# Performance work log

Measured on AMD Instinct MI355X. Metric: run time of the kernel, lower is better.

The kernel has to match this reference:

```python
import jax, jax.numpy as jnp
import numpy as np

N = 100000      # nodes
E = 1600000     # edges (avg degree 16)
IN_DIM = 128
OUT_DIM = 64


def setup_inputs() -> dict:
    key = jax.random.key(0)
    k0, k1, k2, k3, k4 = jax.random.split(key, 5)
    h = jax.random.normal(k0, (N, IN_DIM), dtype=jnp.float32)
    src = jax.random.randint(k1, (E,), 0, N)
    dst = jax.random.randint(k2, (E,), 0, N)
    W = jax.random.normal(k3, (OUT_DIM, IN_DIM), dtype=jnp.float32) * 0.05  # fc.weight
    a = jax.random.normal(k4, (2 * OUT_DIM,), dtype=jnp.float32) * 0.05     # attn_fc.weight (flattened)
    return {"h": h, "src": src, "dst": dst, "W": W, "a": a}


def reference(h, src, dst, W, a):
    # z = fc(h)
    z = h @ W.T                                   # [N, OUT_DIM]
    # attn_fc([z_src, z_dst]) == z_src @ a[:D] + z_dst @ a[D:]  (exact linear split)
    s_src = z @ a[:OUT_DIM]                       # [N]
    s_dst = z @ a[OUT_DIM:]                       # [N]
    e = jax.nn.leaky_relu(s_src[src] + s_dst[dst], negative_slope=0.01)  # [E]
    # segment softmax over incoming edges of each dst node
    m = jax.ops.segment_max(e, dst, num_segments=N)
    m = jnp.where(jnp.isfinite(m), m, 0.0)        # empty segments -> -inf; neutralize
    ee = jnp.exp(e - m[dst])                      # [E]
    denom = jax.ops.segment_sum(ee, dst, num_segments=N)
    alpha = ee / jnp.where(denom == 0, 1.0, denom)[dst]
    # scatter-weighted sum of source features
    h_out = jax.ops.segment_sum(alpha[:, None] * z[src], dst, num_segments=N)  # [N, OUT_DIM]
    # activation = F.elu; residual disabled (in_dim != out_dim * num_heads)
    return jax.nn.elu(h_out)
```

## Files before the change

### kernel.cpp

```cpp
#include <hip/hip_runtime.h>
#include <hip/hip_bf16.h>
#include <math.h>

typedef float floatx4 __attribute__((ext_vector_type(4)));
typedef short short8 __attribute__((ext_vector_type(8)));

#define IN_DIM 128
#define OUT_DIM 64
#define OWNER(d) (((d) >> 4) & 7)
#define CHUNK 2048
#define CAP 32
#define OVF_CAP 8192
#define WPAD 136

__device__ __forceinline__ unsigned short bf16_rne(float f) {
    unsigned u = __float_as_uint(f);
    u += 0x7FFFu + ((u >> 16) & 1u);
    return (unsigned short)(u >> 16);
}
__device__ __forceinline__ float bf16_tof(unsigned short b) {
    return __uint_as_float(((unsigned)b) << 16);
}

__global__ __launch_bounds__(256) void k_gemm(
    const float* __restrict__ h, const float* __restrict__ W,
    const float* __restrict__ a, __hip_bfloat16* __restrict__ z,
    float* __restrict__ s_src, float* __restrict__ s_dst, int N)
{
    __shared__ __align__(16) unsigned short sWhi[64 * WPAD];
    __shared__ __align__(16) unsigned short sWlo[64 * WPAD];

    const int tid = threadIdx.x;
#pragma unroll
    for (int i = 0; i < 32; ++i) {
        int g = tid + 256 * i;
        float f = W[g];
        int row = g >> 7, k = g & 127;
        unsigned short hb = bf16_rne(f);
        sWhi[row * WPAD + k] = hb;
        sWlo[row * WPAD + k] = bf16_rne(f - bf16_tof(hb));
    }

    const int wave = tid >> 6;
    const int l = tid & 63;
    const int lr = l & 15;
    const int lk = l >> 4;
    const int n0w = blockIdx.x * 64 + wave * 16;

    const int arow = min(n0w + lr, N - 1);
    const float* hrow = h + (size_t)arow * IN_DIM;
    short8 ahi[4], alo[4];
#pragma unroll
    for (int ks = 0; ks < 4; ++ks) {
        int k0 = 32 * ks + 8 * lk;
        floatx4 f0 = *(const floatx4*)(hrow + k0);
        floatx4 f1 = *(const floatx4*)(hrow + k0 + 4);
        float fv[8] = {f0.x, f0.y, f0.z, f0.w, f1.x, f1.y, f1.z, f1.w};
#pragma unroll
        for (int j = 0; j < 8; ++j) {
            unsigned short hb = bf16_rne(fv[j]);
            ahi[ks][j] = (short)hb;
            alo[ks][j] = (short)bf16_rne(fv[j] - bf16_tof(hb));
        }
    }
    __syncthreads();

    float ps[4] = {0.f, 0.f, 0.f, 0.f};
    float pd[4] = {0.f, 0.f, 0.f, 0.f};
#pragma unroll
    for (int ct = 0; ct < 4; ++ct) {
        floatx4 acc = (floatx4){0.f, 0.f, 0.f, 0.f};
#pragma unroll
        for (int ks = 0; ks < 4; ++ks) {
            const int boff = (ct * 16 + lr) * WPAD + 32 * ks + 8 * lk;
            short8 bhi = *(const short8*)&sWhi[boff];
            short8 blo = *(const short8*)&sWlo[boff];
            acc = __builtin_amdgcn_mfma_f32_16x16x32_bf16(ahi[ks], bhi, acc, 0, 0, 0);
            acc = __builtin_amdgcn_mfma_f32_16x16x32_bf16(alo[ks], bhi, acc, 0, 0, 0);
            acc = __builtin_amdgcn_mfma_f32_16x16x32_bf16(ahi[ks], blo, acc, 0, 0, 0);
        }
        const float asv = a[ct * 16 + lr];
        const float adv = a[OUT_DIM + ct * 16 + lr];
#pragma unroll
        for (int r = 0; r < 4; ++r) {
            int n = n0w + lk * 4 + r;
            if (n < N)
                z[(size_t)n * OUT_DIM + ct * 16 + lr] = __float2bfloat16(acc[r]);
            ps[r] += acc[r] * asv;
            pd[r] += acc[r] * adv;
        }
    }
#pragma unroll
    for (int r = 0; r < 4; ++r) {
#pragma unroll
        for (int off = 1; off <= 8; off <<= 1) {
            ps[r] += __shfl_xor(ps[r], off);
            pd[r] += __shfl_xor(pd[r], off);
        }
        int n = n0w + lk * 4 + r;
        if (lr == 0 && n < N) {
            s_src[n] = ps[r];
            s_dst[n] = pd[r];
        }
    }
}

__global__ __launch_bounds__(256) void k_scatter(
    const int* __restrict__ src, const int* __restrict__ dst,
    int* __restrict__ cursor, int* __restrict__ ssort,
    int* __restrict__ ovfcnt, int2* __restrict__ ovf, int E)
{
    const int x = blockIdx.x & 7;
    const int c = blockIdx.x >> 3;
    const int e0 = c * CHUNK;
#pragma unroll
    for (int i = 0; i < CHUNK / 256; ++i) {
        int e = e0 + i * 256 + threadIdx.x;
        if (e < E) {
            int d = __builtin_nontemporal_load(&dst[e]);
            if (OWNER(d) == x) {
                int s = __builtin_nontemporal_load(&src[e]);
                int pos = atomicAdd(&cursor[d], 1);
                if (pos < CAP) {
                    ssort[d * CAP + pos] = s;
                } else {
                    int op = atomicAdd(ovfcnt, 1);
                    if (op < OVF_CAP) ovf[op] = make_int2(s, d);
                }
            }
        }
    }
}

__global__ __launch_bounds__(256) void k_node(
    const int* __restrict__ cursor, const int* __restrict__ ssort,
    const float* __restrict__ s_src, const float* __restrict__ s_dst,
    const int* __restrict__ ovfcnt, const int2* __restrict__ ovf,
    const __hip_bfloat16* __restrict__ z, float* __restrict__ out, int N)
{
    const int lane = threadIdx.x & 63;
    const int wave = threadIdx.x >> 6;
    const int n = blockIdx.x * 4 + wave;
    if (n >= N) return;

    const int deg_raw = cursor[n];
    if (deg_raw == 0) {
        __builtin_nontemporal_store(0.f, &out[(size_t)n * OUT_DIM + lane]);
        return;
    }
    const int deg = min(deg_raw, CAP);
    const int base = n * CAP;
    const float sdn = s_dst[n];

    float sum = 0.f;
    float acc = 0.f;
    {
        int kk = lane;
        int sv = 0;
        float ev = 0.f;
        if (kk < deg) {
            sv = __builtin_nontemporal_load(&ssort[base + kk]);
            float sc = s_src[sv] + sdn;
            sc = sc > 0.f ? sc : 0.01f * sc;
            ev = __expf(sc);
        }
        sum += ev;
        for (int j = 0; j < deg; j += 8) {
            float wgt[8], zv[8];
#pragma unroll
            for (int u = 0; u < 8; ++u) {
                int jj = j + u;
                bool ok = jj < deg;
                int s = __shfl(sv, ok ? jj : 0);
                float w = __shfl(ev, ok ? jj : 0);
                wgt[u] = ok ? w : 0.f;
                int sa = ok ? s : 0;
                zv[u] = __bfloat162float(z[(size_t)sa * OUT_DIM + lane]);
            }
#pragma unroll
            for (int u = 0; u < 8; ++u) acc += wgt[u] * zv[u];
        }
    }

    if (deg_raw > CAP) {
        int oc = min(*ovfcnt, OVF_CAP);
        for (int i = 0; i < oc; ++i) {
            int2 p = ovf[i];
            if (p.y == n) {
                float sc = s_src[p.x] + sdn;
                sc = sc > 0.f ? sc : 0.01f * sc;
                float ev = __expf(sc);
                if (lane == 0) sum += ev;
                acc += ev * __bfloat162float(z[(size_t)p.x * OUT_DIM + lane]);
            }
        }
    }

#pragma unroll
    for (int off = 32; off >= 1; off >>= 1) sum += __shfl_xor(sum, off);

    float r = acc / sum;
    float o = r > 0.f ? r : expm1f(r);
    __builtin_nontemporal_store(o, &out[(size_t)n * OUT_DIM + lane]);
}

extern "C" void kernel_launch(void* const* d_in, const int* in_sizes, int n_in,
                              void* d_out, int out_size, void* d_ws, size_t ws_size,
                              hipStream_t stream)
{
    (void)n_in; (void)out_size; (void)ws_size;

    const float* h  = (const float*)d_in[0];
    const int* src  = (const int*)d_in[1];
    const int* dst  = (const int*)d_in[2];
    const float* W  = (const float*)d_in[3];
    const float* a  = (const float*)d_in[4];
    const int N = in_sizes[0] / IN_DIM;
    const int E = in_sizes[1];
    float* out = (float*)d_out;

    char* wsp = (char*)d_ws;
    size_t off = 0;
    auto alloc = [&](size_t bytes) -> void* {
        void* p = wsp + off;
        off = (off + bytes + 255) & ~(size_t)255;
        return p;
    };
    __hip_bfloat16* z = (__hip_bfloat16*)alloc((size_t)N * OUT_DIM * 2);
    float* s_src = (float*)alloc((size_t)N * 4);
    float* s_dst = (float*)alloc((size_t)N * 4);
    int* cursor  = (int*)alloc((size_t)(N + 1) * 4);
    int* ovfcnt  = cursor + N;
    int2* ovf    = (int2*)alloc((size_t)OVF_CAP * 8);
    int* ssort   = (int*)alloc((size_t)N * CAP * 4);

    hipMemsetAsync(cursor, 0, (size_t)(N + 1) * 4, stream);

    const int nchunks = (E + CHUNK - 1) / CHUNK;
    k_gemm<<<(N + 63) / 64, 256, 0, stream>>>(h, W, a, z, s_src, s_dst, N);
    k_scatter<<<nchunks * 8, 256, 0, stream>>>(src, dst, cursor, ssort, ovfcnt, ovf, E);
    k_node<<<(N + 3) / 4, 256, 0, stream>>>(cursor, ssort, s_src, s_dst, ovfcnt, ovf, z, out, N);
}
```

Measured before the change: 245.5 us.

## Fuse projection GEMM and edge scatter into one kernel with interleaved block roles

Merges the feature-projection GEMM and the edge-bucketing scatter into a single launch. Block indices are interleaved so that one in five blocks does GEMM and the rest do scatter, which lets the bandwidth-bound h read overlap with the atomic-heavy scatter and removes one kernel boundary. The GEMM no longer stages W in shared memory; each wave reads W from global memory and splits it into hi/lo bf16 on the fly, which costs extra ALU work and L2 traffic. Node arrays are padded to a multiple of 64, but the clamp means the last tile reads h rows past N, so it reads out of bounds.

```diff
diff --git a/kernel.cpp b/kernel.cpp
--- a/kernel.cpp
+++ b/kernel.cpp
@@ -11,7 +11,6 @@
 #define CHUNK 2048
 #define CAP 32
 #define OVF_CAP 8192
-#define WPAD 136
 
 __device__ __forceinline__ unsigned short bf16_rne(float f) {
     unsigned u = __float_as_uint(f);
@@ -22,110 +21,115 @@
     return __uint_as_float(((unsigned)b) << 16);
 }
 
-__global__ __launch_bounds__(256) void k_gemm(
+__global__ __launch_bounds__(256) void k_front(
     const float* __restrict__ h, const float* __restrict__ W,
     const float* __restrict__ a, __hip_bfloat16* __restrict__ z,
-    float* __restrict__ s_src, float* __restrict__ s_dst, int N)
-{
-    __shared__ __align__(16) unsigned short sWhi[64 * WPAD];
-    __shared__ __align__(16) unsigned short sWlo[64 * WPAD];
-
-    const int tid = threadIdx.x;
-#pragma unroll
-    for (int i = 0; i < 32; ++i) {
-        int g = tid + 256 * i;
-        float f = W[g];
-        int row = g >> 7, k = g & 127;
-        unsigned short hb = bf16_rne(f);
-        sWhi[row * WPAD + k] = hb;
-        sWlo[row * WPAD + k] = bf16_rne(f - bf16_tof(hb));
-    }
-
-    const int wave = tid >> 6;
-    const int l = tid & 63;
-    const int lr = l & 15;
-    const int lk = l >> 4;
-    const int n0w = blockIdx.x * 64 + wave * 16;
-
-    const int arow = min(n0w + lr, N - 1);
-    const float* hrow = h + (size_t)arow * IN_DIM;
-    short8 ahi[4], alo[4];
-#pragma unroll
-    for (int ks = 0; ks < 4; ++ks) {
-        int k0 = 32 * ks + 8 * lk;
-        floatx4 f0 = *(const floatx4*)(hrow + k0);
-        floatx4 f1 = *(const floatx4*)(hrow + k0 + 4);
-        float fv[8] = {f0.x, f0.y, f0.z, f0.w, f1.x, f1.y, f1.z, f1.w};
-#pragma unroll
-        for (int j = 0; j < 8; ++j) {
-            unsigned short hb = bf16_rne(fv[j]);
-            ahi[ks][j] = (short)hb;
-            alo[ks][j] = (short)bf16_rne(fv[j] - bf16_tof(hb));
-        }
-    }
-    __syncthreads();
-
-    float ps[4] = {0.f, 0.f, 0.f, 0.f};
-    float pd[4] = {0.f, 0.f, 0.f, 0.f};
-#pragma unroll
-    for (int ct = 0; ct < 4; ++ct) {
-        floatx4 acc = (floatx4){0.f, 0.f, 0.f, 0.f};
-#pragma unroll
-        for (int ks = 0; ks < 4; ++ks) {
-            const int boff = (ct * 16 + lr) * WPAD + 32 * ks + 8 * lk;
-            short8 bhi = *(const short8*)&sWhi[boff];
-            short8 blo = *(const short8*)&sWlo[boff];
-            acc = __builtin_amdgcn_mfma_f32_16x16x32_bf16(ahi[ks], bhi, acc, 0, 0, 0);
-            acc = __builtin_amdgcn_mfma_f32_16x16x32_bf16(alo[ks], bhi, acc, 0, 0, 0);
-            acc = __builtin_amdgcn_mfma_f32_16x16x32_bf16(ahi[ks], blo, acc, 0, 0, 0);
-        }
-        const float asv = a[ct * 16 + lr];
-        const float adv = a[OUT_DIM + ct * 16 + lr];
-#pragma unroll
-        for (int r = 0; r < 4; ++r) {
-            int n = n0w + lk * 4 + r;
-            if (n < N)
-                z[(size_t)n * OUT_DIM + ct * 16 + lr] = __float2bfloat16(acc[r]);
-            ps[r] += acc[r] * asv;
-            pd[r] += acc[r] * adv;
-        }
-    }
-#pragma unroll
-    for (int r = 0; r < 4; ++r) {
-#pragma unroll
-        for (int off = 1; off <= 8; off <<= 1) {
-            ps[r] += __shfl_xor(ps[r], off);
-            pd[r] += __shfl_xor(pd[r], off);
-        }
-        int n = n0w + lk * 4 + r;
-        if (lr == 0 && n < N) {
-            s_src[n] = ps[r];
-            s_dst[n] = pd[r];
-        }
-    }
-}
-
-__global__ __launch_bounds__(256) void k_scatter(
+    float* __restrict__ s_src, float* __restrict__ s_dst, int nG,
     const int* __restrict__ src, const int* __restrict__ dst,
     int* __restrict__ cursor, int* __restrict__ ssort,
-    int* __restrict__ ovfcnt, int2* __restrict__ ovf, int E)
+    int* __restrict__ ovfcnt, int2* __restrict__ ovf, int E, int nchunks)
 {
-    const int x = blockIdx.x & 7;
-    const int c = blockIdx.x >> 3;
-    const int e0 = c * CHUNK;
-#pragma unroll
-    for (int i = 0; i < CHUNK / 256; ++i) {
-        int e = e0 + i * 256 + threadIdx.x;
-        if (e < E) {
-            int d = __builtin_nontemporal_load(&dst[e]);
-            if (OWNER(d) == x) {
-                int s = __builtin_nontemporal_load(&src[e]);
-                int pos = atomicAdd(&cursor[d], 1);
-                if (pos < CAP) {
-                    ssort[d * CAP + pos] = s;
-                } else {
-                    int op = atomicAdd(ovfcnt, 1);
-                    if (op < OVF_CAP) ovf[op] = make_int2(s, d);
+    const int b = blockIdx.x;
+    const int r = b % 40;
+    const int tid = threadIdx.x;
+
+    if (r % 5 == 0) {
+        const int g = (b / 40) * 8 + r / 5;
+        if (g >= nG) return;
+        const int wave = tid >> 6;
+        const int l = tid & 63;
+        const int lr = l & 15;
+        const int lk = l >> 4;
+        const int n0w = g * 64 + wave * 16;
+
+        const int arow = min(n0w + lr, nG * 64 - 1 < 0 ? 0 : (int)0x7fffffff);
+        (void)arow;
+        const int arow2 = min(n0w + lr, (nG * 64) - 1);
+        const float* hrow = h + (size_t)min(arow2, 0x7fffffff) * IN_DIM;
+        short8 ahi[4], alo[4];
+#pragma unroll
+        for (int ks = 0; ks < 4; ++ks) {
+            int k0 = 32 * ks + 8 * lk;
+            floatx4 f0 = __builtin_nontemporal_load((const floatx4*)(hrow + k0));
+            floatx4 f1 = __builtin_nontemporal_load((const floatx4*)(hrow + k0 + 4));
+            float fv[8] = {f0.x, f0.y, f0.z, f0.w, f1.x, f1.y, f1.z, f1.w};
+#pragma unroll
+            for (int j = 0; j < 8; ++j) {
+                unsigned short hb = bf16_rne(fv[j]);
+                ahi[ks][j] = (short)hb;
+                alo[ks][j] = (short)bf16_rne(fv[j] - bf16_tof(hb));
+            }
+        }
+
+        float ps[4] = {0.f, 0.f, 0.f, 0.f};
+        float pd[4] = {0.f, 0.f, 0.f, 0.f};
+#pragma unroll
+        for (int ct = 0; ct < 4; ++ct) {
+            floatx4 acc = (floatx4){0.f, 0.f, 0.f, 0.f};
+#pragma unroll
+            for (int ks = 0; ks < 4; ++ks) {
+                const float* wrow = W + (ct * 16 + lr) * IN_DIM + 32 * ks + 8 * lk;
+                floatx4 w0 = *(const floatx4*)wrow;
+                floatx4 w1 = *(const floatx4*)(wrow + 4);
+                float wv[8] = {w0.x, w0.y, w0.z, w0.w, w1.x, w1.y, w1.z, w1.w};
+                short8 bhi, blo;
+#pragma unroll
+                for (int j = 0; j < 8; ++j) {
+                    unsigned short hb = bf16_rne(wv[j]);
+                    bhi[j] = (short)hb;
+                    blo[j] = (short)bf16_rne(wv[j] - bf16_tof(hb));
+                }
+                acc = __builtin_amdgcn_mfma_f32_16x16x32_bf16(ahi[ks], bhi, acc, 0, 0, 0);
+                acc = __builtin_amdgcn_mfma_f32_16x16x32_bf16(alo[ks], bhi, acc, 0, 0, 0);
+                acc = __builtin_amdgcn_mfma_f32_16x16x32_bf16(ahi[ks], blo, acc, 0, 0, 0);
+            }
+            const float asv = a[ct * 16 + lr];
+            const float adv = a[OUT_DIM + ct * 16 + lr];
+#pragma unroll
+            for (int rr = 0; rr < 4; ++rr) {
+                int n = n0w + lk * 4 + rr;
+                if (n < nG * 64)
+                    ;
+                ps[rr] += acc[rr] * asv;
+                pd[rr] += acc[rr] * adv;
+                z[(size_t)min(n, nG * 64 - 1) * OUT_DIM + ct * 16 + lr] =
+                    __float2bfloat16(acc[rr]);
+            }
+        }
+#pragma unroll
+        for (int rr = 0; rr < 4; ++rr) {
+#pragma unroll
+            for (int off = 1; off <= 8; off <<= 1) {
+                ps[rr] += __shfl_xor(ps[rr], off);
+                pd[rr] += __shfl_xor(pd[rr], off);
+            }
+            int n = n0w + lk * 4 + rr;
+            if (lr == 0) {
+                s_src[n] = ps[rr];
+                s_dst[n] = pd[rr];
+            }
+        }
+    } else {
+        const int x = r & 7;
+        const int R5v[8] = {0, 25, 10, 35, 20, 5, 30, 15};
+        const int j = (r >> 3) - (R5v[x] < r ? 1 : 0);
+        const int ch = (b / 40) * 4 + j;
+        if (ch >= nchunks) return;
+        const int e0 = ch * CHUNK;
+#pragma unroll
+        for (int i = 0; i < CHUNK / 256; ++i) {
+            int e = e0 + i * 256 + tid;
+            if (e < E) {
+                int d = __builtin_nontemporal_load(&dst[e]);
+                if (OWNER(d) == x) {
+                    int s = __builtin_nontemporal_load(&src[e]);
+                    int pos = atomicAdd(&cursor[d], 1);
+                    if (pos < CAP) {
+                        ssort[d * CAP + pos] = s;
+                    } else {
+                        int op = atomicAdd(ovfcnt, 1);
+                        if (op < OVF_CAP) ovf[op] = make_int2(s, d);
+                    }
                 }
             }
         }
@@ -226,9 +230,10 @@
         off = (off + bytes + 255) & ~(size_t)255;
         return p;
     };
-    __hip_bfloat16* z = (__hip_bfloat16*)alloc((size_t)N * OUT_DIM * 2);
-    float* s_src = (float*)alloc((size_t)N * 4);
-    float* s_dst = (float*)alloc((size_t)N * 4);
+    const int nG = (N + 63) / 64;
+    __hip_bfloat16* z = (__hip_bfloat16*)alloc((size_t)nG * 64 * OUT_DIM * 2);
+    float* s_src = (float*)alloc((size_t)nG * 64 * 4);
+    float* s_dst = (float*)alloc((size_t)nG * 64 * 4);
     int* cursor  = (int*)alloc((size_t)(N + 1) * 4);
     int* ovfcnt  = cursor + N;
     int2* ovf    = (int2*)alloc((size_t)OVF_CAP * 8);
@@ -237,7 +242,12 @@
     hipMemsetAsync(cursor, 0, (size_t)(N + 1) * 4, stream);
 
     const int nchunks = (E + CHUNK - 1) / CHUNK;
-    k_gemm<<<(N + 63) / 64, 256, 0, stream>>>(h, W, a, z, s_src, s_dst, N);
-    k_scatter<<<nchunks * 8, 256, 0, stream>>>(src, dst, cursor, ssort, ovfcnt, ovf, E);
-    k_node<<<(N + 3) / 4, 256, 0, stream>>>(cursor, ssort, s_src, s_dst, ovfcnt, ovf, z, out, N);
-}
+    const int tg = (nG + 7) / 8;
+    const int ts = (nchunks + 3) / 4;
+    const int T = tg > ts ? tg : ts;
+    k_front<<<40 * T, 256, 0, stream>>>(h, W, a, z, s_src, s_dst, nG,
+                                        src, dst, cursor, ssort, ovfcnt, ovf,
+                                        E, nchunks);
+    k_node<<<(N + 3) / 4, 256, 0, stream>>>(cursor, ssort, s_src, s_dst,
+                                            ovfcnt, ovf, z, out, N);
+}
```

Result: slower. 269.5 us (+9.8%).

## Replace global-atomic edge scatter with two-pass bucketed binning via LDS

Applied to the files above, without the earlier changes.

Edge bucketing into per-destination lists now runs in two passes. First, per-chunk blocks bin edges into 256-node buckets using shared-memory atomic counters and pack (src, dst-low-byte) into fixed-capacity cells. Second, one block per bucket fills the per-node lists with LDS cursors. The aim is to replace contended global atomics on cursor[] and the 8x redundant reads of dst with local atomics and more coalesced writes. The cost is an extra intermediate buffer and an extra kernel, plus a spill path that flags overflowed nodes with a high bit in the cursor. The old path remains as a fallback when the workspace is too small.

```diff
diff --git a/kernel.cpp b/kernel.cpp
--- a/kernel.cpp
+++ b/kernel.cpp
@@ -12,6 +12,10 @@
 #define CAP 32
 #define OVF_CAP 8192
 #define WPAD 136
+#define NB_SHIFT 8
+#define CELL_CAP 24
+#define CHUNK1 4096
+#define SPILL_BIT (1 << 20)
 
 __device__ __forceinline__ unsigned short bf16_rne(float f) {
     unsigned u = __float_as_uint(f);
@@ -102,6 +106,79 @@
             s_src[n] = ps[r];
             s_dst[n] = pd[r];
         }
+    }
+}
+
+__global__ __launch_bounds__(256) void k_bin(
+    const int* __restrict__ src, const int* __restrict__ dst,
+    int* __restrict__ cursor, unsigned* __restrict__ bdata,
+    int* __restrict__ bcnt, int* __restrict__ ovfcnt,
+    int2* __restrict__ ovf, int E, int NB)
+{
+    __shared__ int cell[512];
+    const int tid = threadIdx.x;
+    for (int i = tid; i < NB; i += 256) cell[i] = 0;
+    __syncthreads();
+
+    const int c = blockIdx.x;
+    const int e0 = c * CHUNK1;
+    const size_t cbase = (size_t)c * NB * CELL_CAP;
+#pragma unroll
+    for (int i = 0; i < CHUNK1 / 256; ++i) {
+        int e = e0 + i * 256 + tid;
+        if (e < E) {
+            int d = __builtin_nontemporal_load(&dst[e]);
+            int s = __builtin_nontemporal_load(&src[e]);
+            int b = d >> NB_SHIFT;
+            int slot = atomicAdd(&cell[b], 1);
+            if (slot < CELL_CAP) {
+                bdata[cbase + (size_t)b * CELL_CAP + slot] =
+                    ((unsigned)s << 8) | (unsigned)(d & 255);
+            } else {
+                atomicAdd(&cursor[d], SPILL_BIT);
+                int op = atomicAdd(ovfcnt, 1);
+                if (op < OVF_CAP) ovf[op] = make_int2(s, d);
+            }
+        }
+    }
+    __syncthreads();
+    for (int b = tid; b < NB; b += 256) bcnt[c * NB + b] = cell[b];
+}
+
+__global__ __launch_bounds__(256) void k_fill(
+    const unsigned* __restrict__ bdata, const int* __restrict__ bcnt,
+    int* __restrict__ cursor, int* __restrict__ ssort,
+    int* __restrict__ ovfcnt, int2* __restrict__ ovf,
+    int nb1, int NB, int N)
+{
+    __shared__ int lcur[256];
+    const int tid = threadIdx.x;
+    lcur[tid] = 0;
+    __syncthreads();
+
+    const int b = blockIdx.x;
+    const int n0 = b << NB_SHIFT;
+    for (int c = tid; c < nb1; c += 256) {
+        int cnt = min(bcnt[c * NB + b], CELL_CAP);
+        size_t base = ((size_t)c * NB + b) * CELL_CAP;
+        for (int j = 0; j < cnt; ++j) {
+            unsigned v = bdata[base + j];
+            int i = (int)(v & 255u);
+            int s = (int)(v >> 8);
+            int slot = atomicAdd(&lcur[i], 1);
+            if (slot < CAP) {
+                ssort[(n0 + i) * CAP + slot] = s;
+            } else {
+                int op = atomicAdd(ovfcnt, 1);
+                if (op < OVF_CAP) ovf[op] = make_int2(s, n0 + i);
+            }
+        }
+    }
+    __syncthreads();
+    int n = n0 + tid;
+    if (n < N) {
+        int v = lcur[tid];
+        if (v) cursor[n] += v;
     }
 }
 
@@ -143,12 +220,13 @@
     const int n = blockIdx.x * 4 + wave;
     if (n >= N) return;
 
-    const int deg_raw = cursor[n];
-    if (deg_raw == 0) {
+    const int raw = cursor[n];
+    if (raw == 0) {
         __builtin_nontemporal_store(0.f, &out[(size_t)n * OUT_DIM + lane]);
         return;
     }
-    const int deg = min(deg_raw, CAP);
+    const int low = raw & 0xFFFFF;
+    const int deg = min(low, CAP);
     const int base = n * CAP;
     const float sdn = s_dst[n];
 
@@ -182,7 +260,7 @@
         }
     }
 
-    if (deg_raw > CAP) {
+    if (raw > CAP) {
         int oc = min(*ovfcnt, OVF_CAP);
         for (int i = 0; i < oc; ++i) {
             int2 p = ovf[i];
@@ -208,7 +286,7 @@
                               void* d_out, int out_size, void* d_ws, size_t ws_size,
                               hipStream_t stream)
 {
-    (void)n_in; (void)out_size; (void)ws_size;
+    (void)n_in; (void)out_size;
 
     const float* h  = (const float*)d_in[0];
     const int* src  = (const int*)d_in[1];
@@ -218,6 +296,17 @@
     const int N = in_sizes[0] / IN_DIM;
     const int E = in_sizes[1];
     float* out = (float*)d_out;
+
+    const int NB  = (N + 255) >> NB_SHIFT;
+    const int nb1 = (E + CHUNK1 - 1) / CHUNK1;
+
+    auto rnd = [](size_t b) { return (b + 255) & ~(size_t)255; };
+    const size_t meta_ints = (size_t)NB * 256 + 1 + (size_t)nb1 * NB;
+    const size_t need_bucket =
+        rnd((size_t)N * OUT_DIM * 2) + 2 * rnd((size_t)N * 4) +
+        rnd(meta_ints * 4) + rnd((size_t)OVF_CAP * 8) +
+        rnd((size_t)N * CAP * 4) + rnd((size_t)nb1 * NB * CELL_CAP * 4);
+    const bool bucketed = (NB <= 512) && (need_bucket <= ws_size);
 
     char* wsp = (char*)d_ws;
     size_t off = 0;
@@ -229,15 +318,35 @@
     __hip_bfloat16* z = (__hip_bfloat16*)alloc((size_t)N * OUT_DIM * 2);
     float* s_src = (float*)alloc((size_t)N * 4);
     float* s_dst = (float*)alloc((size_t)N * 4);
-    int* cursor  = (int*)alloc((size_t)(N + 1) * 4);
-    int* ovfcnt  = cursor + N;
-    int2* ovf    = (int2*)alloc((size_t)OVF_CAP * 8);
-    int* ssort   = (int*)alloc((size_t)N * CAP * 4);
-
-    hipMemsetAsync(cursor, 0, (size_t)(N + 1) * 4, stream);
 
     const int nchunks = (E + CHUNK - 1) / CHUNK;
     k_gemm<<<(N + 63) / 64, 256, 0, stream>>>(h, W, a, z, s_src, s_dst, N);
-    k_scatter<<<nchunks * 8, 256, 0, stream>>>(src, dst, cursor, ssort, ovfcnt, ovf, E);
-    k_node<<<(N + 3) / 4, 256, 0, stream>>>(cursor, ssort, s_src, s_dst, ovfcnt, ovf, z, out, N);
-}
+
+    if (bucketed) {
+        int* cursor = (int*)alloc(meta_ints * 4);
+        int* ovfcnt = cursor + (size_t)NB * 256;
+        int* bcnt   = ovfcnt + 1;
+        int2* ovf   = (int2*)alloc((size_t)OVF_CAP * 8);
+        int* ssort  = (int*)alloc((size_t)N * CAP * 4);
+        unsigned* bdata = (unsigned*)alloc((size_t)nb1 * NB * CELL_CAP * 4);
+
+        hipMemsetAsync(cursor, 0, meta_ints * 4, stream);
+        k_bin<<<nb1, 256, 0, stream>>>(src, dst, cursor, bdata, bcnt,
+                                       ovfcnt, ovf, E, NB);
+        k_fill<<<NB, 256, 0, stream>>>(bdata, bcnt, cursor, ssort,
+                                       ovfcnt, ovf, nb1, NB, N);
+        k_node<<<(N + 3) / 4, 256, 0, stream>>>(cursor, ssort, s_src, s_dst,
+                                                ovfcnt, ovf, z, out, N);
+    } else {
+        int* cursor = (int*)alloc((size_t)(N + 1) * 4);
+        int* ovfcnt = cursor + N;
+        int2* ovf   = (int2*)alloc((size_t)OVF_CAP * 8);
+        int* ssort  = (int*)alloc((size_t)N * CAP * 4);
+
+        hipMemsetAsync(cursor, 0, (size_t)(N + 1) * 4, stream);
+        k_scatter<<<nchunks * 8, 256, 0, stream>>>(src, dst, cursor, ssort,
+                                                   ovfcnt, ovf, E);
+        k_node<<<(N + 3) / 4, 256, 0, stream>>>(cursor, ssort, s_src, s_dst,
+                                                ovfcnt, ovf, z, out, N);
+    }
+}
```

After: 221.2 us. -9.9%, faster.
